# Kernel tuning notes

Measured on AMD Instinct MI355X. Metric: run time of the kernel, lower is better.

Reference implementation:

```python
import jax, jax.numpy as jnp
import numpy as np

N_NODES = 100000
N_HYPER = 20000
N_EDGES = 1600000
D = 128


def layer_norm(x, gamma, beta, eps=1e-5):
    mu = jnp.mean(x, axis=-1, keepdims=True)
    var = jnp.mean(jnp.square(x - mu), axis=-1, keepdims=True)
    return (x - mu) * jax.lax.rsqrt(var + eps) * gamma + beta


def setup_inputs() -> dict:
    key = jax.random.key(0)
    ks = jax.random.split(key, 12)
    s = 1.0 / np.sqrt(D)
    s4 = 1.0 / np.sqrt(4 * D)
    return {
        "h": jax.random.normal(ks[0], (N_NODES, D), jnp.float32),
        "src": jax.random.randint(ks[1], (N_EDGES,), 0, N_NODES),
        "dst": jax.random.randint(ks[2], (N_EDGES,), 0, N_HYPER),
        # node->hyperedge GraphConv
        "W1": jax.random.normal(ks[3], (D, D), jnp.float32) * s,
        "b1": jnp.zeros((D,), jnp.float32),
        # hyperedge->node GraphConv
        "W2": jax.random.normal(ks[4], (D, D), jnp.float32) * s,
        "b2": jnp.zeros((D,), jnp.float32),
        # FFN
        "W3": jax.random.normal(ks[5], (D, 4 * D), jnp.float32) * s,
        "b3": jnp.zeros((4 * D,), jnp.float32),
        "W4": jax.random.normal(ks[6], (4 * D, D), jnp.float32) * s4,
        "b4": jnp.zeros((D,), jnp.float32),
        # LayerNorms
        "gamma1": jnp.ones((D,), jnp.float32),
        "beta1": jnp.zeros((D,), jnp.float32),
        "gamma2": jnp.ones((D,), jnp.float32),
        "beta2": jnp.zeros((D,), jnp.float32),
    }


def reference(h, src, dst, W1, b1, W2, b2, W3, b3, W4, b4,
              gamma1, beta1, gamma2, beta2):
    ones_e = jnp.ones((N_EDGES,), h.dtype)
    # symmetric GraphConv norms (DGL norm='both', degrees clamped to >= 1)
    deg_node = jnp.maximum(jax.ops.segment_sum(ones_e, src, N_NODES), 1.0)
    deg_he = jnp.maximum(jax.ops.segment_sum(ones_e, dst, N_HYPER), 1.0)
    cn = jax.lax.rsqrt(deg_node)[:, None]  # [N_NODES,1]
    ch = jax.lax.rsqrt(deg_he)[:, None]    # [N_HYPER,1]

    # node -> hyperedge: h_hyper = D_he^{-1/2} A^T D_node^{-1/2} h W1 + b1
    msg = (h * cn)[src]                                  # [E, D]
    h_hyper = jax.ops.segment_sum(msg, dst, N_HYPER) * ch
    h_hyper = h_hyper @ W1 + b1                          # [N_HYPER, D]

    # hyperedge -> node on reversed graph (same norms, swapped roles)
    msg2 = (h_hyper * ch)[dst]                           # [E, D]
    h_node = jax.ops.segment_sum(msg2, src, N_NODES) * cn
    h_node = h_node @ W2 + b2                            # [N_NODES, D]

    # residual + LN, FFN + residual + LN (dropout = identity in eval)
    h1 = layer_norm(h + h_node, gamma1, beta1)
    ffn = jax.nn.relu(h1 @ W3 + b3) @ W4 + b4
    return layer_norm(h1 + ffn, gamma2, beta2)
```

## Files before the change

kernel.cpp:

```cpp
#include <hip/hip_runtime.h>

#define N_NODES 100000
#define N_HYPER 20000
#define N_EDGES 1600000
#define LDW 136

#define NB_HE 79
#define NB_ND 391
#define CHUNK 6250

typedef unsigned short u16;
typedef unsigned int u32;
typedef short bf16x8 __attribute__((ext_vector_type(8)));
typedef float f32x4 __attribute__((ext_vector_type(4)));

__device__ __forceinline__ f32x4 mfma16(bf16x8 a, bf16x8 b, f32x4 c) {
    return __builtin_amdgcn_mfma_f32_16x16x32_bf16(a, b, c, 0, 0, 0);
}
__device__ __forceinline__ u16 f2bf(float f) {
    unsigned u = __float_as_uint(f);
    unsigned r = u + 0x7FFFu + ((u >> 16) & 1u);
    return (u16)(r >> 16);
}
__device__ __forceinline__ void bfu(unsigned v, float& f0, float& f1) {
    f0 = __uint_as_float(v << 16);
    f1 = __uint_as_float(v & 0xFFFF0000u);
}

__global__ __launch_bounds__(256) void k_prep(const float* __restrict__ W1, const float* __restrict__ W2,
                                              const float* __restrict__ W3, const float* __restrict__ W4,
                                              u16* __restrict__ W1t, u16* __restrict__ W2t,
                                              u16* __restrict__ W3t, u16* __restrict__ W4t,
                                              const float* __restrict__ h, u16* __restrict__ h_bf) {
    int i = blockIdx.x * 256 + threadIdx.x;
    if (i < 16384) {
        int k = i & 127, n = i >> 7;
        W1t[n * 128 + k] = f2bf(W1[k * 128 + n]);
        W2t[n * 128 + k] = f2bf(W2[k * 128 + n]);
    }
    if (i < 65536) {
        int k = i & 127, n = i >> 7;
        W3t[n * 128 + k] = f2bf(W3[k * 512 + n]);
        int k4 = i & 511, n4 = i >> 9;
        W4t[n4 * 512 + k4] = f2bf(W4[k4 * 128 + n4]);
    }
    if (i < 3276800) {
        float4 v = ((const float4*)h)[i];
        uint2 st;
        st.x = (u32)f2bf(v.x) | ((u32)f2bf(v.y) << 16);
        st.y = (u32)f2bf(v.z) | ((u32)f2bf(v.w) << 16);
        ((uint2*)h_bf)[i] = st;
    }
}

__global__ __launch_bounds__(256) void k_bin_hist(const int* __restrict__ src, const int* __restrict__ dst,
                                                  int* __restrict__ bkt_he, int* __restrict__ bkt_nd) {
    __shared__ int hh[NB_HE], hn[NB_ND];
    int t = threadIdx.x;
    for (int i = t; i < NB_HE; i += 256) hh[i] = 0;
    for (int i = t; i < NB_ND; i += 256) hn[i] = 0;
    __syncthreads();
    int e0 = blockIdx.x * CHUNK;
    for (int e = e0 + t; e < e0 + CHUNK; e += 256) {
        atomicAdd(&hn[src[e] >> 8], 1);
        atomicAdd(&hh[dst[e] >> 8], 1);
    }
    __syncthreads();
    for (int i = t; i < NB_HE; i += 256) if (hh[i]) atomicAdd(&bkt_he[i], hh[i]);
    for (int i = t; i < NB_ND; i += 256) if (hn[i]) atomicAdd(&bkt_nd[i], hn[i]);
}

__global__ __launch_bounds__(512) void k_bin_scan(int* __restrict__ bkt_he, int* __restrict__ bkt_nd,
                                                  int* __restrict__ start_he, int* __restrict__ start_nd,
                                                  int* __restrict__ ptr_node, int* __restrict__ ptr_he) {
    __shared__ int sc[512];
    int t = threadIdx.x;
    int vhe = (t < NB_HE) ? bkt_he[t] : 0;
    sc[t] = vhe; __syncthreads();
    for (int off = 1; off < 512; off <<= 1) {
        int v = (t >= off) ? sc[t - off] : 0; __syncthreads();
        sc[t] += v; __syncthreads();
    }
    if (t < NB_HE) { int ex = sc[t] - vhe; start_he[t] = ex; bkt_he[t] = ex; }
    if (t == NB_HE - 1) start_he[NB_HE] = sc[t];
    __syncthreads();
    int vnd = (t < NB_ND) ? bkt_nd[t] : 0;
    sc[t] = vnd; __syncthreads();
    for (int off = 1; off < 512; off <<= 1) {
        int v = (t >= off) ? sc[t - off] : 0; __syncthreads();
        sc[t] += v; __syncthreads();
    }
    if (t < NB_ND) { int ex = sc[t] - vnd; start_nd[t] = ex; bkt_nd[t] = ex; }
    if (t == NB_ND - 1) start_nd[NB_ND] = sc[t];
    if (t == 0) { ptr_node[N_NODES] = N_EDGES; ptr_he[N_HYPER] = N_EDGES; }
}

__global__ __launch_bounds__(256) void k_bin_fill(const int* __restrict__ src, const int* __restrict__ dst,
                                                  int* __restrict__ bkt_he, int* __restrict__ bkt_nd,
                                                  u32* __restrict__ bin_he, u32* __restrict__ bin_nd) {
    __shared__ int hh[NB_HE], hn[NB_ND], bh[NB_HE], bn[NB_ND];
    int t = threadIdx.x;
    for (int i = t; i < NB_HE; i += 256) hh[i] = 0;
    for (int i = t; i < NB_ND; i += 256) hn[i] = 0;
    __syncthreads();
    int e0 = blockIdx.x * CHUNK;
    for (int e = e0 + t; e < e0 + CHUNK; e += 256) {
        atomicAdd(&hn[src[e] >> 8], 1);
        atomicAdd(&hh[dst[e] >> 8], 1);
    }
    __syncthreads();
    for (int i = t; i < NB_HE; i += 256) { int c = hh[i]; bh[i] = c ? atomicAdd(&bkt_he[i], c) : 0; }
    for (int i = t; i < NB_ND; i += 256) { int c = hn[i]; bn[i] = c ? atomicAdd(&bkt_nd[i], c) : 0; }
    __syncthreads();
    for (int i = t; i < NB_HE; i += 256) hh[i] = 0;
    for (int i = t; i < NB_ND; i += 256) hn[i] = 0;
    __syncthreads();
    for (int e = e0 + t; e < e0 + CHUNK; e += 256) {
        int s = src[e], d = dst[e];
        int bd = d >> 8, bs_ = s >> 8;
        int ph = bh[bd] + atomicAdd(&hh[bd], 1);
        bin_he[ph] = ((u32)(d & 255) << 24) | (u32)s;
        int pn = bn[bs_] + atomicAdd(&hn[bs_], 1);
        bin_nd[pn] = ((u32)(s & 255) << 24) | (u32)d;
    }
}

__global__ __launch_bounds__(256) void k_deg(const u32* __restrict__ bin_he, const u32* __restrict__ bin_nd,
                                             const int* __restrict__ start_he, const int* __restrict__ start_nd,
                                             int* __restrict__ deg_nd, int* __restrict__ deg_he) {
    __shared__ int cnt[256];
    int t = threadIdx.x, b = blockIdx.x;
    cnt[t] = 0; __syncthreads();
    if (b < NB_HE) {
        int lo = start_he[b], hi = start_he[b + 1];
        for (int j = lo + t; j < hi; j += 256) atomicAdd(&cnt[bin_he[j] >> 24], 1);
        __syncthreads();
        int id = b * 256 + t;
        if (id < N_HYPER) deg_he[id] = cnt[t];
    } else {
        int bb = b - NB_HE;
        int lo = start_nd[bb], hi = start_nd[bb + 1];
        for (int j = lo + t; j < hi; j += 256) atomicAdd(&cnt[bin_nd[j] >> 24], 1);
        __syncthreads();
        int id = bb * 256 + t;
        if (id < N_NODES) deg_nd[id] = cnt[t];
    }
}

__global__ __launch_bounds__(256) void k_scanA(const int* __restrict__ a_node,
                                               const int* __restrict__ a_he,
                                               int* __restrict__ bs) {
    __shared__ int red[256];
    int b = blockIdx.x;
    const int* a; int base, n;
    if (b < 25) { a = a_node; base = b * 4096; n = N_NODES; }
    else        { a = a_he;   base = (b - 25) * 4096; n = N_HYPER; }
    int t = threadIdx.x;
    int lo = base + t * 16;
    int s = 0;
#pragma unroll
    for (int i = 0; i < 16; ++i) {
        int idx = lo + i;
        if (idx < n) s += a[idx];
    }
    red[t] = s;
    __syncthreads();
    for (int off = 128; off > 0; off >>= 1) {
        if (t < off) red[t] += red[t + off];
        __syncthreads();
    }
    if (t == 0) bs[b] = red[0];
}

__global__ void k_scanB(int* __restrict__ bs) {
    int t = threadIdx.x;
    if (t == 0) {
        int run = 0;
        for (int i = 0; i < 25; ++i) { int v = bs[i]; bs[i] = run; run += v; }
    } else if (t == 1) {
        int run = 0;
        for (int i = 25; i < 30; ++i) { int v = bs[i]; bs[i] = run; run += v; }
    }
}

__global__ __launch_bounds__(256) void k_scanC(int* __restrict__ a_node, int* __restrict__ a_he,
                                               float* __restrict__ iq_node, float* __restrict__ iq_he,
                                               const int* __restrict__ bs) {
    __shared__ int pre[256];
    int b = blockIdx.x;
    int* a; float* iq; int base, n;
    if (b < 25) { a = a_node; iq = iq_node; base = b * 4096; n = N_NODES; }
    else        { a = a_he;   iq = iq_he;   base = (b - 25) * 4096; n = N_HYPER; }
    int t = threadIdx.x;
    int lo = base + t * 16;
    int loc = 0;
#pragma unroll
    for (int i = 0; i < 16; ++i) { int idx = lo + i; if (idx < n) loc += a[idx]; }
    pre[t] = loc;
    __syncthreads();
    for (int off = 1; off < 256; off <<= 1) {
        int v = (t >= off) ? pre[t - off] : 0;
        __syncthreads();
        pre[t] += v;
        __syncthreads();
    }
    int running = bs[b] + pre[t] - loc;
#pragma unroll
    for (int i = 0; i < 16; ++i) {
        int idx = lo + i;
        if (idx < n) {
            int d = a[idx];
            iq[idx] = rsqrtf((float)(d < 1 ? 1 : d));
            a[idx] = running;
            running += d;
        }
    }
}

__global__ __launch_bounds__(256) void k_fill2(const u32* __restrict__ bin_he, const u32* __restrict__ bin_nd,
                                               const int* __restrict__ start_he, const int* __restrict__ start_nd,
                                               const int* __restrict__ ptr_he, const int* __restrict__ ptr_node,
                                               int* __restrict__ adj_he, int* __restrict__ adj_node) {
    __shared__ int base[256], rk[256];
    int t = threadIdx.x, b = blockIdx.x;
    rk[t] = 0;
    if (b < NB_HE) {
        int id = b * 256 + t;
        base[t] = (id < N_HYPER) ? ptr_he[id] : 0;
        __syncthreads();
        int lo = start_he[b], hi = start_he[b + 1];
        for (int j = lo + t; j < hi; j += 256) {
            u32 v = bin_he[j];
            int lid = v >> 24;
            int pos = base[lid] + atomicAdd(&rk[lid], 1);
            adj_he[pos] = (int)(v & 0xFFFFFFu);
        }
    } else {
        int bb = b - NB_HE;
        int id = bb * 256 + t;
        base[t] = (id < N_NODES) ? ptr_node[id] : 0;
        __syncthreads();
        int lo = start_nd[bb], hi = start_nd[bb + 1];
        for (int j = lo + t; j < hi; j += 256) {
            u32 v = bin_nd[j];
            int lid = v >> 24;
            int pos = base[lid] + atomicAdd(&rk[lid], 1);
            adj_node[pos] = (int)(v & 0xFFFFFFu);
        }
    }
}

__global__ __launch_bounds__(256) void k_gather1(const u16* __restrict__ h_bf,
                                                 const int* __restrict__ adj,
                                                 const int* __restrict__ ptr,
                                                 const float* __restrict__ cn,
                                                 float* __restrict__ acc1) {
    int row = blockIdx.x * 4 + (threadIdx.x >> 6);
    int lane = threadIdx.x & 63;
    int p = lane >> 5, c = lane & 31;
    int start = ptr[row];
    int end = ptr[row + 1];
    const uint2* hp = (const uint2*)h_bf;
    float A0[4] = {0, 0, 0, 0}, A1[4] = {0, 0, 0, 0};
    float f0, f1, f2, f3;
    int j = start;
    for (; j + 3 < end; j += 4) {
        int sA = adj[j + p], sB = adj[j + 2 + p];
        float wA = cn[sA], wB = cn[sB];
        uint2 vA = hp[sA * 32 + c];
        uint2 vB = hp[sB * 32 + c];
        bfu(vA.x, f0, f1); bfu(vA.y, f2, f3);
        A0[0] += f0 * wA; A0[1] += f1 * wA; A0[2] += f2 * wA; A0[3] += f3 * wA;
        bfu(vB.x, f0, f1); bfu(vB.y, f2, f3);
        A1[0] += f0 * wB; A1[1] += f1 * wB; A1[2] += f2 * wB; A1[3] += f3 * wB;
    }
    for (; j + 1 < end; j += 2) {
        int sA = adj[j + p];
        float wA = cn[sA];
        uint2 vA = hp[sA * 32 + c];
        bfu(vA.x, f0, f1); bfu(vA.y, f2, f3);
        A0[0] += f0 * wA; A0[1] += f1 * wA; A0[2] += f2 * wA; A0[3] += f3 * wA;
    }
    if (j < end && p == 0) {
        int sA = adj[j];
        float wA = cn[sA];
        uint2 vA = hp[sA * 32 + c];
        bfu(vA.x, f0, f1); bfu(vA.y, f2, f3);
        A0[0] += f0 * wA; A0[1] += f1 * wA; A0[2] += f2 * wA; A0[3] += f3 * wA;
    }
    float r0 = A0[0] + A1[0], r1 = A0[1] + A1[1], r2 = A0[2] + A1[2], r3 = A0[3] + A1[3];
    r0 += __shfl_xor(r0, 32, 64);
    r1 += __shfl_xor(r1, 32, 64);
    r2 += __shfl_xor(r2, 32, 64);
    r3 += __shfl_xor(r3, 32, 64);
    if (p == 0) {
        float4 o; o.x = r0; o.y = r1; o.z = r2; o.w = r3;
        ((float4*)acc1)[row * 32 + c] = o;
    }
}

__global__ __launch_bounds__(256) void k_gather2(const u16* __restrict__ hh2b,
                                                 const int* __restrict__ adj,
                                                 const int* __restrict__ ptr,
                                                 float* __restrict__ acc2) {
    int row = blockIdx.x * 4 + (threadIdx.x >> 6);
    int lane = threadIdx.x & 63;
    int p = lane >> 5, c = lane & 31;
    int start = ptr[row];
    int end = ptr[row + 1];
    const uint2* hp = (const uint2*)hh2b;
    float A0[4] = {0, 0, 0, 0}, A1[4] = {0, 0, 0, 0};
    float f0, f1, f2, f3;
    int j = start;
    for (; j + 3 < end; j += 4) {
        int dA = adj[j + p], dB = adj[j + 2 + p];
        uint2 vA = hp[dA * 32 + c];
        uint2 vB = hp[dB * 32 + c];
        bfu(vA.x, f0, f1); bfu(vA.y, f2, f3);
        A0[0] += f0; A0[1] += f1; A0[2] += f2; A0[3] += f3;
        bfu(vB.x, f0, f1); bfu(vB.y, f2, f3);
        A1[0] += f0; A1[1] += f1; A1[2] += f2; A1[3] += f3;
    }
    for (; j + 1 < end; j += 2) {
        int dA = adj[j + p];
        uint2 vA = hp[dA * 32 + c];
        bfu(vA.x, f0, f1); bfu(vA.y, f2, f3);
        A0[0] += f0; A0[1] += f1; A0[2] += f2; A0[3] += f3;
    }
    if (j < end && p == 0) {
        int dA = adj[j];
        uint2 vA = hp[dA * 32 + c];
        bfu(vA.x, f0, f1); bfu(vA.y, f2, f3);
        A0[0] += f0; A0[1] += f1; A0[2] += f2; A0[3] += f3;
    }
    float r0 = A0[0] + A1[0], r1 = A0[1] + A1[1], r2 = A0[2] + A1[2], r3 = A0[3] + A1[3];
    r0 += __shfl_xor(r0, 32, 64);
    r1 += __shfl_xor(r1, 32, 64);
    r2 += __shfl_xor(r2, 32, 64);
    r3 += __shfl_xor(r3, 32, 64);
    if (p == 0) {
        float4 o; o.x = r0; o.y = r1; o.z = r2; o.w = r3;
        ((float4*)acc2)[row * 32 + c] = o;
    }
}

__global__ __launch_bounds__(256) void k_gemm1(const float* __restrict__ a, const float* __restrict__ ch,
                                               const u16* __restrict__ W1t,
                                               const float* __restrict__ b1,
                                               u16* __restrict__ hh2b) {
    __shared__ u16 sA[64 * LDW];
    __shared__ u16 sW[128 * LDW];
    int tid = threadIdx.x;
    int r0 = blockIdx.x * 64;
    for (int i = tid; i < 64 * 32; i += 256) {
        int r = i >> 5, c4 = i & 31;
        int row = r0 + r; if (row > N_HYPER - 1) row = N_HYPER - 1;
        float4 v = *(const float4*)(a + row * 128 + c4 * 4);
        float cw = ch[row];
        u16* p = &sA[r * LDW + c4 * 4];
        p[0] = f2bf(v.x * cw); p[1] = f2bf(v.y * cw);
        p[2] = f2bf(v.z * cw); p[3] = f2bf(v.w * cw);
    }
    for (int i = tid; i < 128 * 16; i += 256) {
        int n = i >> 4, c = i & 15;
        *(uint4*)&sW[n * LDW + c * 8] = *(const uint4*)(W1t + n * 128 + c * 8);
    }
    __syncthreads();
    int w = tid >> 6, l15 = tid & 15, quad = (tid & 63) >> 4;
    f32x4 zero = {0.f, 0.f, 0.f, 0.f};
    f32x4 acc[8];
#pragma unroll
    for (int nt = 0; nt < 8; ++nt) acc[nt] = zero;
    int arow = w * 16 + l15;
#pragma unroll
    for (int kt = 0; kt < 4; ++kt) {
        bf16x8 af = *(bf16x8*)&sA[arow * LDW + kt * 32 + quad * 8];
#pragma unroll
        for (int nt = 0; nt < 8; ++nt) {
            bf16x8 bfv = *(bf16x8*)&sW[(nt * 16 + l15) * LDW + kt * 32 + quad * 8];
            acc[nt] = mfma16(af, bfv, acc[nt]);
        }
    }
#pragma unroll
    for (int r = 0; r < 4; ++r) {
        int row = r0 + w * 16 + quad * 4 + r;
        if (row < N_HYPER) {
            float cw = ch[row];
#pragma unroll
            for (int nt = 0; nt < 8; ++nt) {
                int n = nt * 16 + l15;
                hh2b[row * 128 + n] = f2bf((acc[nt][r] + b1[n]) * cw);
            }
        }
    }
}

__global__ __launch_bounds__(256) void k_gemm2_ln(float* a, const float* __restrict__ cn,
                                                  const u16* __restrict__ W2t,
                                                  const float* __restrict__ b2,
                                                  const float* __restrict__ h,
                                                  const float* __restrict__ gamma1,
                                                  const float* __restrict__ beta1) {
    __shared__ u16 sA[64 * LDW];
    __shared__ u16 sW[128 * LDW];
    int tid = threadIdx.x;
    int r0 = blockIdx.x * 64;
    for (int i = tid; i < 64 * 32; i += 256) {
        int r = i >> 5, c4 = i & 31;
        int row = r0 + r; if (row > N_NODES - 1) row = N_NODES - 1;
        float4 v = *(const float4*)(a + row * 128 + c4 * 4);
        float cw = cn[row];
        u16* p = &sA[r * LDW + c4 * 4];
        p[0] = f2bf(v.x * cw); p[1] = f2bf(v.y * cw);
        p[2] = f2bf(v.z * cw); p[3] = f2bf(v.w * cw);
    }
    for (int i = tid; i < 128 * 16; i += 256) {
        int n = i >> 4, c = i & 15;
        *(uint4*)&sW[n * LDW + c * 8] = *(const uint4*)(W2t + n * 128 + c * 8);
    }
    __syncthreads();
    int w = tid >> 6, l15 = tid & 15, quad = (tid & 63) >> 4;
    f32x4 zero = {0.f, 0.f, 0.f, 0.f};
    f32x4 acc[8];
#pragma unroll
    for (int nt = 0; nt < 8; ++nt) acc[nt] = zero;
    int arow = w * 16 + l15;
#pragma unroll
    for (int kt = 0; kt < 4; ++kt) {
        bf16x8 af = *(bf16x8*)&sA[arow * LDW + kt * 32 + quad * 8];
#pragma unroll
        for (int nt = 0; nt < 8; ++nt) {
            bf16x8 bfv = *(bf16x8*)&sW[(nt * 16 + l15) * LDW + kt * 32 + quad * 8];
            acc[nt] = mfma16(af, bfv, acc[nt]);
        }
    }
    float s1[4] = {0, 0, 0, 0}, s2[4] = {0, 0, 0, 0};
#pragma unroll
    for (int r = 0; r < 4; ++r) {
        int row = r0 + w * 16 + quad * 4 + r;
        int rc = row > N_NODES - 1 ? N_NODES - 1 : row;
#pragma unroll
        for (int nt = 0; nt < 8; ++nt) {
            int n = nt * 16 + l15;
            float t = acc[nt][r] + b2[n] + h[rc * 128 + n];
            acc[nt][r] = t;
            s1[r] += t; s2[r] += t * t;
        }
    }
#pragma unroll
    for (int off = 1; off < 16; off <<= 1) {
#pragma unroll
        for (int r = 0; r < 4; ++r) {
            s1[r] += __shfl_xor(s1[r], off, 64);
            s2[r] += __shfl_xor(s2[r], off, 64);
        }
    }
#pragma unroll
    for (int r = 0; r < 4; ++r) {
        int row = r0 + w * 16 + quad * 4 + r;
        if (row < N_NODES) {
            float mu = s1[r] * (1.f / 128.f);
            float var = s2[r] * (1.f / 128.f) - mu * mu;
            float rs = rsqrtf(var + 1e-5f);
#pragma unroll
            for (int nt = 0; nt < 8; ++nt) {
                int n = nt * 16 + l15;
                a[row * 128 + n] = (acc[nt][r] - mu) * rs * gamma1[n] + beta1[n];
            }
        }
    }
}

__global__ __launch_bounds__(256) void k_ffn_ln(const float* __restrict__ h1,
                                                const u16* __restrict__ W3t,
                                                const float* __restrict__ b3,
                                                const u16* __restrict__ W4t,
                                                const float* __restrict__ b4,
                                                const float* __restrict__ gamma2,
                                                const float* __restrict__ beta2,
                                                float* __restrict__ out) {
    __shared__ u16 sA[64 * LDW];
    __shared__ u16 sW[128 * LDW];
    __shared__ u16 sY[64 * LDW];
    int tid = threadIdx.x;
    int r0 = blockIdx.x * 64;
    for (int i = tid; i < 64 * 32; i += 256) {
        int r = i >> 5, c4 = i & 31;
        int row = r0 + r; if (row > N_NODES - 1) row = N_NODES - 1;
        float4 v = *(const float4*)(h1 + row * 128 + c4 * 4);
        u16* p = &sA[r * LDW + c4 * 4];
        p[0] = f2bf(v.x); p[1] = f2bf(v.y); p[2] = f2bf(v.z); p[3] = f2bf(v.w);
    }
    int w = tid >> 6, l15 = tid & 15, quad = (tid & 63) >> 4;
    int arow = w * 16 + l15;
    f32x4 zero = {0.f, 0.f, 0.f, 0.f};
    f32x4 acc[8];
#pragma unroll
    for (int nt = 0; nt < 8; ++nt) acc[nt] = zero;

    for (int nc = 0; nc < 4; ++nc) {
        __syncthreads();
        for (int i = tid; i < 128 * 16; i += 256) {
            int n = i >> 4, c = i & 15;
            *(uint4*)&sW[n * LDW + c * 8] = *(const uint4*)(W3t + (nc * 128 + n) * 128 + c * 8);
        }
        __syncthreads();
        f32x4 y[8];
#pragma unroll
        for (int nt = 0; nt < 8; ++nt) y[nt] = zero;
#pragma unroll
        for (int kt = 0; kt < 4; ++kt) {
            bf16x8 af = *(bf16x8*)&sA[arow * LDW + kt * 32 + quad * 8];
#pragma unroll
            for (int nt = 0; nt < 8; ++nt) {
                bf16x8 bfv = *(bf16x8*)&sW[(nt * 16 + l15) * LDW + kt * 32 + quad * 8];
                y[nt] = mfma16(af, bfv, y[nt]);
            }
        }
#pragma unroll
        for (int r = 0; r < 4; ++r) {
            int yrow = w * 16 + quad * 4 + r;
#pragma unroll
            for (int nt = 0; nt < 8; ++nt) {
                int n = nt * 16 + l15;
                float vv = y[nt][r] + b3[nc * 128 + n];
                sY[yrow * LDW + n] = f2bf(vv > 0.f ? vv : 0.f);
            }
        }
        __syncthreads();
        for (int i = tid; i < 128 * 16; i += 256) {
            int n = i >> 4, c = i & 15;
            *(uint4*)&sW[n * LDW + c * 8] = *(const uint4*)(W4t + n * 512 + nc * 128 + c * 8);
        }
        __syncthreads();
#pragma unroll
        for (int kt = 0; kt < 4; ++kt) {
            bf16x8 af = *(bf16x8*)&sY[arow * LDW + kt * 32 + quad * 8];
#pragma unroll
            for (int nt = 0; nt < 8; ++nt) {
                bf16x8 bfv = *(bf16x8*)&sW[(nt * 16 + l15) * LDW + kt * 32 + quad * 8];
                acc[nt] = mfma16(af, bfv, acc[nt]);
            }
        }
    }
    float s1[4] = {0, 0, 0, 0}, s2[4] = {0, 0, 0, 0};
#pragma unroll
    for (int r = 0; r < 4; ++r) {
        int row = r0 + w * 16 + quad * 4 + r;
        int rc = row > N_NODES - 1 ? N_NODES - 1 : row;
#pragma unroll
        for (int nt = 0; nt < 8; ++nt) {
            int n = nt * 16 + l15;
            float t = acc[nt][r] + b4[n] + h1[rc * 128 + n];
            acc[nt][r] = t;
            s1[r] += t; s2[r] += t * t;
        }
    }
#pragma unroll
    for (int off = 1; off < 16; off <<= 1) {
#pragma unroll
        for (int r = 0; r < 4; ++r) {
            s1[r] += __shfl_xor(s1[r], off, 64);
            s2[r] += __shfl_xor(s2[r], off, 64);
        }
    }
#pragma unroll
    for (int r = 0; r < 4; ++r) {
        int row = r0 + w * 16 + quad * 4 + r;
        if (row < N_NODES) {
            float mu = s1[r] * (1.f / 128.f);
            float var = s2[r] * (1.f / 128.f) - mu * mu;
            float rs = rsqrtf(var + 1e-5f);
#pragma unroll
            for (int nt = 0; nt < 8; ++nt) {
                int n = nt * 16 + l15;
                out[row * 128 + n] = (acc[nt][r] - mu) * rs * gamma2[n] + beta2[n];
            }
        }
    }
}

extern "C" void kernel_launch(void* const* d_in, const int* in_sizes, int n_in,
                              void* d_out, int out_size, void* d_ws, size_t ws_size,
                              hipStream_t stream) {
    const float* h      = (const float*)d_in[0];
    const int*   src    = (const int*)d_in[1];
    const int*   dst    = (const int*)d_in[2];
    const float* W1     = (const float*)d_in[3];
    const float* b1     = (const float*)d_in[4];
    const float* W2     = (const float*)d_in[5];
    const float* b2     = (const float*)d_in[6];
    const float* W3     = (const float*)d_in[7];
    const float* b3     = (const float*)d_in[8];
    const float* W4     = (const float*)d_in[9];
    const float* b4     = (const float*)d_in[10];
    const float* gamma1 = (const float*)d_in[11];
    const float* beta1  = (const float*)d_in[12];
    const float* gamma2 = (const float*)d_in[13];
    const float* beta2  = (const float*)d_in[14];
    float* out = (float*)d_out;

    char* ws = (char*)d_ws;
    int*   ptr_node = (int*)(ws + 0);
    int*   ptr_he   = (int*)(ws + 400512);
    int*   adj_he   = (int*)(ws + 481280);
    int*   adj_node = (int*)(ws + 6881280);
    float* cn       = (float*)(ws + 13281280);
    float* ch       = (float*)(ws + 13681280);
    u16*   h_bf     = (u16*)(ws + 24000000);
    u32*   bin_he   = (u32*)(ws + 49600000);
    u32*   bin_nd   = (u32*)(ws + 56000000);
    float* acc1     = (float*)(ws + 62400000);
    int*   bkt_he   = (int*)(ws + 72640000);
    int*   bkt_nd   = (int*)(ws + 72640512);
    int*   start_he = (int*)(ws + 72642560);
    int*   start_nd = (int*)(ws + 72643072);
    int*   bs       = (int*)(ws + 72644864);
    float* acc2     = (float*)(ws + 24000000);
    u16*   hh2b     = (u16*)(ws + 481280);
    u16*   W1t      = (u16*)(ws + 75200000);
    u16*   W2t      = (u16*)(ws + 75232768);
    u16*   W3t      = (u16*)(ws + 75265536);
    u16*   W4t      = (u16*)(ws + 75396608);

    hipMemsetAsync(ws + 72640000, 0, 2560, stream);

    k_prep<<<12800, 256, 0, stream>>>(W1, W2, W3, W4, W1t, W2t, W3t, W4t, h, h_bf);
    k_bin_hist<<<256, 256, 0, stream>>>(src, dst, bkt_he, bkt_nd);
    k_bin_scan<<<1, 512, 0, stream>>>(bkt_he, bkt_nd, start_he, start_nd, ptr_node, ptr_he);
    k_bin_fill<<<256, 256, 0, stream>>>(src, dst, bkt_he, bkt_nd, bin_he, bin_nd);
    k_deg<<<NB_HE + NB_ND, 256, 0, stream>>>(bin_he, bin_nd, start_he, start_nd, ptr_node, ptr_he);
    k_scanA<<<30, 256, 0, stream>>>(ptr_node, ptr_he, bs);
    k_scanB<<<1, 64, 0, stream>>>(bs);
    k_scanC<<<30, 256, 0, stream>>>(ptr_node, ptr_he, cn, ch, bs);
    k_fill2<<<NB_HE + NB_ND, 256, 0, stream>>>(bin_he, bin_nd, start_he, start_nd,
                                               ptr_he, ptr_node, adj_he, adj_node);
    k_gather1<<<5000, 256, 0, stream>>>(h_bf, adj_he, ptr_he, cn, acc1);
    k_gemm1<<<313, 256, 0, stream>>>(acc1, ch, W1t, b1, hh2b);
    k_gather2<<<25000, 256, 0, stream>>>(hh2b, adj_node, ptr_node, acc2);
    k_gemm2_ln<<<1563, 256, 0, stream>>>(acc2, cn, W2t, b2, h, gamma1, beta1);
    k_ffn_ln<<<1563, 256, 0, stream>>>(acc2, W3t, b3, W4t, b4, gamma2, beta2, out);
}
```

Before: 517.4 us.

## Restructure FFN kernel to 128-row tiles with weights read directly from global

```diff
diff --git a/kernel.cpp b/kernel.cpp
--- a/kernel.cpp
+++ b/kernel.cpp
@@ -479,105 +479,122 @@
                                                 const float* __restrict__ gamma2,
                                                 const float* __restrict__ beta2,
                                                 float* __restrict__ out) {
-    __shared__ u16 sA[64 * LDW];
-    __shared__ u16 sW[128 * LDW];
-    __shared__ u16 sY[64 * LDW];
+    __shared__ u16 sA[128 * LDW];
+    __shared__ u16 sY[128 * LDW];
     int tid = threadIdx.x;
-    int r0 = blockIdx.x * 64;
-    for (int i = tid; i < 64 * 32; i += 256) {
-        int r = i >> 5, c4 = i & 31;
+    int w = tid >> 6, lane = tid & 63;
+    int l15 = lane & 15, quad = lane >> 4;
+    int r0 = blockIdx.x * 128;
+    for (int i = lane; i < 32 * 32; i += 64) {
+        int r = w * 32 + (i >> 5), c4 = i & 31;
         int row = r0 + r; if (row > N_NODES - 1) row = N_NODES - 1;
         float4 v = *(const float4*)(h1 + row * 128 + c4 * 4);
-        u16* p = &sA[r * LDW + c4 * 4];
-        p[0] = f2bf(v.x); p[1] = f2bf(v.y); p[2] = f2bf(v.z); p[3] = f2bf(v.w);
-    }
-    int w = tid >> 6, l15 = tid & 15, quad = (tid & 63) >> 4;
-    int arow = w * 16 + l15;
+        uint2 st;
+        st.x = (u32)f2bf(v.x) | ((u32)f2bf(v.y) << 16);
+        st.y = (u32)f2bf(v.z) | ((u32)f2bf(v.w) << 16);
+        *(uint2*)&sA[r * LDW + c4 * 4] = st;
+    }
+    __builtin_amdgcn_sched_barrier(0);
+
+    int a0 = w * 32 + l15, a1 = a0 + 16;
     f32x4 zero = {0.f, 0.f, 0.f, 0.f};
-    f32x4 acc[8];
-#pragma unroll
-    for (int nt = 0; nt < 8; ++nt) acc[nt] = zero;
+    f32x4 acc[2][8];
+#pragma unroll
+    for (int s = 0; s < 2; ++s)
+#pragma unroll
+        for (int nt = 0; nt < 8; ++nt) acc[s][nt] = zero;
 
     for (int nc = 0; nc < 4; ++nc) {
-        __syncthreads();
-        for (int i = tid; i < 128 * 16; i += 256) {
-            int n = i >> 4, c = i & 15;
-            *(uint4*)&sW[n * LDW + c * 8] = *(const uint4*)(W3t + (nc * 128 + n) * 128 + c * 8);
-        }
-        __syncthreads();
-        f32x4 y[8];
-#pragma unroll
-        for (int nt = 0; nt < 8; ++nt) y[nt] = zero;
+        f32x4 y[2][8];
+#pragma unroll
+        for (int s = 0; s < 2; ++s)
+#pragma unroll
+            for (int nt = 0; nt < 8; ++nt) y[s][nt] = zero;
 #pragma unroll
         for (int kt = 0; kt < 4; ++kt) {
-            bf16x8 af = *(bf16x8*)&sA[arow * LDW + kt * 32 + quad * 8];
+            bf16x8 af0 = *(bf16x8*)&sA[a0 * LDW + kt * 32 + quad * 8];
+            bf16x8 af1 = *(bf16x8*)&sA[a1 * LDW + kt * 32 + quad * 8];
+            const u16* wp = W3t + (nc * 128 + l15) * 128 + kt * 32 + quad * 8;
 #pragma unroll
             for (int nt = 0; nt < 8; ++nt) {
-                bf16x8 bfv = *(bf16x8*)&sW[(nt * 16 + l15) * LDW + kt * 32 + quad * 8];
-                y[nt] = mfma16(af, bfv, y[nt]);
-            }
-        }
+                bf16x8 bv = *(const bf16x8*)(wp + nt * 16 * 128);
+                y[0][nt] = mfma16(af0, bv, y[0][nt]);
+                y[1][nt] = mfma16(af1, bv, y[1][nt]);
+            }
+        }
+#pragma unroll
+        for (int nt = 0; nt < 8; ++nt) {
+            float bb = b3[nc * 128 + nt * 16 + l15];
+#pragma unroll
+            for (int s = 0; s < 2; ++s) {
+                int mb = w * 32 + s * 16 + quad * 4;
+#pragma unroll
+                for (int r = 0; r < 4; ++r) {
+                    float vv = y[s][nt][r] + bb;
+                    sY[(mb + r) * LDW + nt * 16 + l15] = f2bf(vv > 0.f ? vv : 0.f);
+                }
+            }
+        }
+        __builtin_amdgcn_sched_barrier(0);
+#pragma unroll
+        for (int kt = 0; kt < 4; ++kt) {
+            bf16x8 ay0 = *(bf16x8*)&sY[a0 * LDW + kt * 32 + quad * 8];
+            bf16x8 ay1 = *(bf16x8*)&sY[a1 * LDW + kt * 32 + quad * 8];
+            const u16* wp4 = W4t + l15 * 512 + nc * 128 + kt * 32 + quad * 8;
+#pragma unroll
+            for (int nt = 0; nt < 8; ++nt) {
+                bf16x8 bv = *(const bf16x8*)(wp4 + nt * 16 * 512);
+                acc[0][nt] = mfma16(ay0, bv, acc[0][nt]);
+                acc[1][nt] = mfma16(ay1, bv, acc[1][nt]);
+            }
+        }
+        __builtin_amdgcn_sched_barrier(0);
+    }
+    float s1[2][4], s2[2][4];
+#pragma unroll
+    for (int s = 0; s < 2; ++s)
+#pragma unroll
+        for (int r = 0; r < 4; ++r) { s1[s][r] = 0.f; s2[s][r] = 0.f; }
+#pragma unroll
+    for (int s = 0; s < 2; ++s)
 #pragma unroll
         for (int r = 0; r < 4; ++r) {
-            int yrow = w * 16 + quad * 4 + r;
+            int row = r0 + w * 32 + s * 16 + quad * 4 + r;
+            int rc = row > N_NODES - 1 ? N_NODES - 1 : row;
 #pragma unroll
             for (int nt = 0; nt < 8; ++nt) {
                 int n = nt * 16 + l15;
-                float vv = y[nt][r] + b3[nc * 128 + n];
-                sY[yrow * LDW + n] = f2bf(vv > 0.f ? vv : 0.f);
-            }
-        }
-        __syncthreads();
-        for (int i = tid; i < 128 * 16; i += 256) {
-            int n = i >> 4, c = i & 15;
-            *(uint4*)&sW[n * LDW + c * 8] = *(const uint4*)(W4t + n * 512 + nc * 128 + c * 8);
-        }
-        __syncthreads();
-#pragma unroll
-        for (int kt = 0; kt < 4; ++kt) {
-            bf16x8 af = *(bf16x8*)&sY[arow * LDW + kt * 32 + quad * 8];
-#pragma unroll
-            for (int nt = 0; nt < 8; ++nt) {
-                bf16x8 bfv = *(bf16x8*)&sW[(nt * 16 + l15) * LDW + kt * 32 + quad * 8];
-                acc[nt] = mfma16(af, bfv, acc[nt]);
-            }
-        }
-    }
-    float s1[4] = {0, 0, 0, 0}, s2[4] = {0, 0, 0, 0};
-#pragma unroll
-    for (int r = 0; r < 4; ++r) {
-        int row = r0 + w * 16 + quad * 4 + r;
-        int rc = row > N_NODES - 1 ? N_NODES - 1 : row;
-#pragma unroll
-        for (int nt = 0; nt < 8; ++nt) {
-            int n = nt * 16 + l15;
-            float t = acc[nt][r] + b4[n] + h1[rc * 128 + n];
-            acc[nt][r] = t;
-            s1[r] += t; s2[r] += t * t;
-        }
-    }
+                float t = acc[s][nt][r] + b4[n] + h1[rc * 128 + n];
+                acc[s][nt][r] = t;
+                s1[s][r] += t; s2[s][r] += t * t;
+            }
+        }
 #pragma unroll
     for (int off = 1; off < 16; off <<= 1) {
 #pragma unroll
+        for (int s = 0; s < 2; ++s)
+#pragma unroll
+            for (int r = 0; r < 4; ++r) {
+                s1[s][r] += __shfl_xor(s1[s][r], off, 64);
+                s2[s][r] += __shfl_xor(s2[s][r], off, 64);
+            }
+    }
+#pragma unroll
+    for (int s = 0; s < 2; ++s)
+#pragma unroll
         for (int r = 0; r < 4; ++r) {
-            s1[r] += __shfl_xor(s1[r], off, 64);
-            s2[r] += __shfl_xor(s2[r], off, 64);
-        }
-    }
-#pragma unroll
-    for (int r = 0; r < 4; ++r) {
-        int row = r0 + w * 16 + quad * 4 + r;
-        if (row < N_NODES) {
-            float mu = s1[r] * (1.f / 128.f);
-            float var = s2[r] * (1.f / 128.f) - mu * mu;
-            float rs = rsqrtf(var + 1e-5f);
-#pragma unroll
-            for (int nt = 0; nt < 8; ++nt) {
-                int n = nt * 16 + l15;
-                out[row * 128 + n] = (acc[nt][r] - mu) * rs * gamma2[n] + beta2[n];
-            }
-        }
-    }
+            int row = r0 + w * 32 + s * 16 + quad * 4 + r;
+            if (row < N_NODES) {
+                float mu = s1[s][r] * (1.f / 128.f);
+                float var = s2[s][r] * (1.f / 128.f) - mu * mu;
+                float rs = rsqrtf(var + 1e-5f);
+#pragma unroll
+                for (int nt = 0; nt < 8; ++nt) {
+                    int n = nt * 16 + l15;
+                    out[row * 128 + n] = (acc[s][nt][r] - mu) * rs * gamma2[n] + beta2[n];
+                }
+            }
+        }
 }
 
 extern "C" void kernel_launch(void* const* d_in, const int* in_sizes, int n_in,
@@ -639,5 +656,5 @@
     k_gemm1<<<313, 256, 0, stream>>>(acc1, ch, W1t, b1, hh2b);
     k_gather2<<<25000, 256, 0, stream>>>(hh2b, adj_node, ptr_node, acc2);
     k_gemm2_ln<<<1563, 256, 0, stream>>>(acc2, cn, W2t, b2, h, gamma1, beta1);
-    k_ffn_ln<<<1563, 256, 0, stream>>>(acc2, W3t, b3, W4t, b4, gamma2, beta2, out);
-}
+    k_ffn_ln<<<782, 256, 0, stream>>>(acc2, W3t, b3, W4t, b4, gamma2, beta2, out);
+}
```

After: 562.5 us. 8.7% more time.
